# Kernel optimization log

Measured on AMD Instinct MI355X. Metric: run time of the kernel, lower is better.

Reference implementation:

```python
import jax, jax.numpy as jnp
import numpy as np

N = 4096      # total nodes (target + context)
T = 1024      # target nodes
C = N - T     # context nodes
F = 128       # raw node feature dim
H = 512       # num_hids
HEADS = 16    # num_heads
D = H // HEADS
WIN = 2       # window_size
L = 2         # num_layers
E_T = 65536   # edges: target queries -> context keys
E_C = 98304   # edges: context queries -> target keys
EDGE_ENC = 8
EDGE_DIST = 8
SCALE = D ** -0.5


def setup_inputs():
    key = jax.random.key(0)
    ks = iter(jax.random.split(key, 40))
    s = 0.02
    rn = lambda shp, sc=1.0: jax.random.normal(next(ks), shp, jnp.float32) * sc
    return {
        "node_feats": rn((N, F)),
        "edge_emb_table": rn((EDGE_ENC * WIN, H), s),
        "edge_dist_emb_table": rn((EDGE_DIST, H), s),
        "w_node": rn((F, H), s), "b_node": jnp.zeros((H,), jnp.float32),
        "w_edge_enc": rn((H, HEADS), s), "b_edge_enc": jnp.zeros((HEADS,), jnp.float32),
        "w_edge_dist": rn((H, HEADS), s), "b_edge_dist": jnp.zeros((HEADS,), jnp.float32),
        "ln1_g": jnp.ones((L, H), jnp.float32), "ln1_b": jnp.zeros((L, H), jnp.float32),
        "attn1_w": rn((L, 4, H, H), s), "attn1_b": jnp.zeros((L, 4, H), jnp.float32),
        "attn2_w": rn((L, 4, H, H), s), "attn2_b": jnp.zeros((L, 4, H), jnp.float32),
        "ln2_g": jnp.ones((L, H), jnp.float32), "ln2_b": jnp.zeros((L, H), jnp.float32),
        "ffn_w1": rn((L, H, H), s), "ffn_b1": jnp.zeros((L, H), jnp.float32),
        "ffn_w2": rn((L, H, H), s), "ffn_b2": jnp.zeros((L, H), jnp.float32),
        "edge_encodes": jax.random.randint(next(ks), (N, N, WIN), 0, EDGE_ENC * WIN, jnp.int32),
        "edge_dist_encodes": jax.random.randint(next(ks), (N, N), 0, EDGE_DIST, jnp.int32),
        "target_sparse_row": jax.random.randint(next(ks), (E_T,), 0, T, jnp.int32),
        "target_sparse_col": jax.random.randint(next(ks), (E_T,), 0, C, jnp.int32),
        "context_sparse_row": jax.random.randint(next(ks), (E_C,), 0, C, jnp.int32),
        "context_sparse_col": jax.random.randint(next(ks), (E_C,), 0, T, jnp.int32),
        "target_node_size": T,
    }


def _ln(x, g, b, eps=1e-5):
    m = jnp.mean(x, -1, keepdims=True)
    v = jnp.mean((x - m) ** 2, -1, keepdims=True)
    return (x - m) * jax.lax.rsqrt(v + eps) * g + b


def _seg_softmax(x, idx, n):
    # scatter-max / scatter-sum softmax over edges grouped by row index
    m = jax.ops.segment_max(x, idx, num_segments=n)
    m = jnp.where(jnp.isfinite(m), m, 0.0)  # empty segments
    e = jnp.exp(x - m[idx])
    s = jax.ops.segment_sum(e, idx, num_segments=n)
    return e / (s[idx] + 1e-16)


def _emb(table, idx):
    # nn.Embedding(max_norm=True): looked-up rows renormed to L2 norm <= 1
    e = table[idx]
    nrm = jnp.linalg.norm(e, axis=-1, keepdims=True)
    return e / jnp.maximum(nrm, 1.0)


def _mha(yq, ykv, w, b, bias, row, col, n_out):
    # w: [4,H,H] = q,k,v,o projections; b: [4,H]
    q = (yq @ w[0] + b[0]).reshape(-1, HEADS, D)
    k = (ykv @ w[1] + b[1]).reshape(-1, HEADS, D)
    v = (ykv @ w[2] + b[2]).reshape(-1, HEADS, D)
    s = jnp.einsum('ehd,ehd->eh', q[row], k[col]) * SCALE + bias  # [E,HEADS]
    a = _seg_softmax(s, row, n_out)
    o = jax.ops.segment_sum(a[:, :, None] * v[col], row, num_segments=n_out)
    return o.reshape(-1, H) @ w[3] + b[3]


def _forward(node_feats, edge_emb_table, edge_dist_emb_table, w_node, b_node,
             w_edge_enc, b_edge_enc, w_edge_dist, b_edge_dist,
             ln1_g, ln1_b, attn1_w, attn1_b, attn2_w, attn2_b,
             ln2_g, ln2_b, ffn_w1, ffn_b1, ffn_w2, ffn_b2,
             edge_encodes, edge_dist_encodes,
             target_sparse_row, target_sparse_col,
             context_sparse_row, context_sparse_col, Tn):
    Cn = node_feats.shape[0] - Tn

    def bias_for(rows, cols):
        # get_encodings: mean over window of edge embedding, plus dist embedding
        e1 = jnp.mean(_emb(edge_emb_table, edge_encodes[rows, cols]), axis=-2)  # [E,H]
        b1 = e1 @ w_edge_enc + b_edge_enc
        e2 = _emb(edge_dist_emb_table, edge_dist_encodes[rows, cols])           # [E,H]
        b2 = e2 @ w_edge_dist + b_edge_dist
        return b1 + b2                                                           # [E,HEADS]

    attn_bias_target = bias_for(target_sparse_row, target_sparse_col + Tn)
    attn_bias_context = bias_for(context_sparse_row + Tn, context_sparse_col)

    x = node_feats @ w_node + b_node
    for l in range(L):
        y = _ln(x, ln1_g[l], ln1_b[l])
        y_t, y_c = y[:Tn], y[Tn:]
        out1 = _mha(y_t, y_c, attn1_w[l], attn1_b[l], attn_bias_target,
                    target_sparse_row, target_sparse_col, Tn)    # [T,H]
        out2 = _mha(y_c, y_t, attn2_w[l], attn2_b[l], attn_bias_context,
                    context_sparse_row, context_sparse_col, Cn)  # [C,H]
        # original code: y_all = cat([y_target_, y_context_]) = [attn2 out, attn1 out]
        x = x + jnp.concatenate([out2, out1], axis=0)
        y = _ln(x, ln2_g[l], ln2_b[l])
        y = jax.nn.gelu(y @ ffn_w1[l] + ffn_b1[l], approximate=False) @ ffn_w2[l] + ffn_b2[l]
        x = x + y
    return x


def reference(node_feats, edge_emb_table, edge_dist_emb_table, w_node, b_node,
              w_edge_enc, b_edge_enc, w_edge_dist, b_edge_dist,
              ln1_g, ln1_b, attn1_w, attn1_b, attn2_w, attn2_b,
              ln2_g, ln2_b, ffn_w1, ffn_b1, ffn_w2, ffn_b2,
              edge_encodes, edge_dist_encodes,
              target_sparse_row, target_sparse_col,
              context_sparse_row, context_sparse_col, target_node_size):
    return _forward(node_feats, edge_emb_table, edge_dist_emb_table, w_node, b_node,
                    w_edge_enc, b_edge_enc, w_edge_dist, b_edge_dist,
                    ln1_g, ln1_b, attn1_w, attn1_b, attn2_w, attn2_b,
                    ln2_g, ln2_b, ffn_w1, ffn_b1, ffn_w2, ffn_b2,
                    edge_encodes, edge_dist_encodes,
                    target_sparse_row, target_sparse_col,
                    context_sparse_row, context_sparse_col, target_node_size)
```

## Files before the change

### kernel.cpp

```cpp
#include <hip/hip_runtime.h>
#include <math.h>

#define N_NODES 4096
#define T_NODES 1024
#define C_NODES 3072
#define F_IN    128
#define H_DIM   512
#define HEADS   16
#define D_HEAD  32
#define E_T     65536
#define E_C     98304
#define SCALE_QK 0.17677669529663687f

typedef __attribute__((ext_vector_type(8))) short short8;
typedef __attribute__((ext_vector_type(4))) float f32x4;

struct ushort4_t { unsigned short x, y, z, w; };

__device__ inline unsigned short f2bf(float f) {
    unsigned u = __float_as_uint(f);
    unsigned r = (u + 0x7fffu + ((u >> 16) & 1u)) >> 16;
    return (unsigned short)r;
}
__device__ inline float bf2f(unsigned short u) {
    return __uint_as_float(((unsigned)u) << 16);
}

__device__ inline void gload16(const void* g, void* l) {
    __builtin_amdgcn_global_load_lds(
        (const __attribute__((address_space(1))) unsigned int*)g,
        (__attribute__((address_space(3))) unsigned int*)l, 16, 0, 0);
}

struct TD { const float* src[20]; unsigned short* dst[20]; };

__global__ void prep_kernel(TD d, const float* __restrict__ w_node, unsigned short* __restrict__ wnT,
                            const float* __restrict__ nf, unsigned short* __restrict__ nfb)
{
    int z = blockIdx.z;
    __shared__ float tile[32][33];
    int tr = threadIdx.x >> 5, tc = threadIdx.x & 31;
    if (z < 20) {
        const float* src = d.src[z];
        unsigned short* dst = d.dst[z];
        int r0 = blockIdx.y * 32, c0 = blockIdx.x * 32;
        #pragma unroll
        for (int p = 0; p < 4; ++p) tile[tr + 8*p][tc] = src[(size_t)(r0 + tr + 8*p)*512 + c0 + tc];
        __syncthreads();
        #pragma unroll
        for (int p = 0; p < 4; ++p) dst[(size_t)(c0 + tr + 8*p)*512 + r0 + tc] = f2bf(tile[tc][tr + 8*p]);
    } else if (z == 20) {
        if (blockIdx.y >= 4) return;
        int r0 = blockIdx.y * 32, c0 = blockIdx.x * 32;
        #pragma unroll
        for (int p = 0; p < 4; ++p) tile[tr + 8*p][tc] = w_node[(size_t)(r0 + tr + 8*p)*512 + c0 + tc];
        __syncthreads();
        #pragma unroll
        for (int p = 0; p < 4; ++p) wnT[(size_t)(c0 + tr + 8*p)*128 + r0 + tc] = f2bf(tile[tc][tr + 8*p]);
    } else {
        int gid = (blockIdx.y * 16 + blockIdx.x) * 256 + threadIdx.x;
        #pragma unroll
        for (int rep = 0; rep < 2; ++rep) {
            int i = gid + rep * 65536;
            float4 v = ((const float4*)nf)[i];
            ushort4_t o = { f2bf(v.x), f2bf(v.y), f2bf(v.z), f2bf(v.w) };
            ((ushort4_t*)nfb)[i] = o;
        }
    }
}

__global__ void proj_kernel(const float* __restrict__ emb, const float* __restrict__ dist_emb,
                            const float* __restrict__ w_enc, const float* __restrict__ w_dist,
                            const float* __restrict__ a1b, const float* __restrict__ a2b,
                            float* __restrict__ P1, float* __restrict__ P2,
                            float* __restrict__ bct, float* __restrict__ bcc)
{
    if (blockIdx.x == 96) {
        int t = threadIdx.x;
        for (int l = 0; l < 2; ++l)
            for (int i = t; i < 512; i += 256) {
                bct[l*1536 + i]        = a1b[(l*4+0)*512 + i];
                bct[l*1536 + 512 + i]  = a2b[(l*4+1)*512 + i];
                bct[l*1536 + 1024 + i] = a2b[(l*4+2)*512 + i];
                bcc[l*1536 + i]        = a1b[(l*4+1)*512 + i];
                bcc[l*1536 + 512 + i]  = a1b[(l*4+2)*512 + i];
                bcc[l*1536 + 1024 + i] = a2b[(l*4+0)*512 + i];
            }
        return;
    }
    int wid = threadIdx.x >> 6, lane = threadIdx.x & 63;
    int o = blockIdx.x * 4 + wid;
    const float* src; const float* wm; float* dst; int h;
    if (o < 256) { src = emb      + (size_t)(o >> 4) * 512; wm = w_enc;  h = o & 15;  dst = P1 + o; }
    else { int o2 = o - 256; src = dist_emb + (size_t)(o2 >> 4) * 512; wm = w_dist; h = o2 & 15; dst = P2 + o2; }
    float4 v0 = ((const float4*)src)[lane*2];
    float4 v1 = ((const float4*)src)[lane*2+1];
    float nrm = v0.x*v0.x + v0.y*v0.y + v0.z*v0.z + v0.w*v0.w
              + v1.x*v1.x + v1.y*v1.y + v1.z*v1.z + v1.w*v1.w;
    int f0 = lane * 8;
    float dt = v0.x*wm[(f0+0)*16+h] + v0.y*wm[(f0+1)*16+h] + v0.z*wm[(f0+2)*16+h] + v0.w*wm[(f0+3)*16+h]
             + v1.x*wm[(f0+4)*16+h] + v1.y*wm[(f0+5)*16+h] + v1.z*wm[(f0+6)*16+h] + v1.w*wm[(f0+7)*16+h];
    #pragma unroll
    for (int s = 1; s < 64; s <<= 1) { nrm += __shfl_xor(nrm, s, 64); dt += __shfl_xor(dt, s, 64); }
    if (lane == 0) *dst = dt / fmaxf(sqrtf(nrm), 1.0f);
}

__global__ void hist2_kernel(const int* __restrict__ t_row, const int* __restrict__ c_row,
                             int* __restrict__ cnt_t, int* __restrict__ cnt_c) {
    int i = blockIdx.x * 256 + threadIdx.x;
    if (i < E_T) atomicAdd(&cnt_t[t_row[i]], 1);
    else atomicAdd(&cnt_c[c_row[i - E_T]], 1);
}

__global__ void scan2_kernel(const int* __restrict__ cnt_t, int* __restrict__ off_t, int* __restrict__ cur_t,
                             const int* __restrict__ cnt_c, int* __restrict__ off_c, int* __restrict__ cur_c) {
    const int* counts; int* offsets; int* cursor; int n;
    if (blockIdx.x == 0) { counts = cnt_t; offsets = off_t; cursor = cur_t; n = T_NODES; }
    else                 { counts = cnt_c; offsets = off_c; cursor = cur_c; n = C_NODES; }
    __shared__ int lds[1024];
    int t = threadIdx.x;
    int c = (n + 1023) / 1024;
    int base = t * c;
    int s = 0;
    for (int j = 0; j < c; ++j) { int i = base + j; if (i < n) s += counts[i]; }
    lds[t] = s;
    __syncthreads();
    for (int d = 1; d < 1024; d <<= 1) {
        int v = (t >= d) ? lds[t-d] : 0;
        __syncthreads();
        lds[t] += v;
        __syncthreads();
    }
    int run = lds[t] - s;
    for (int j = 0; j < c; ++j) {
        int i = base + j;
        if (i < n) { offsets[i] = run; cursor[i] = run; run += counts[i]; }
    }
    if (t == 1023) offsets[n] = lds[1023];
}

__global__ void scatter2_kernel(const int* __restrict__ t_row, const int* __restrict__ c_row,
                                int* __restrict__ cur_t, int* __restrict__ cur_c,
                                int* __restrict__ perm_t, int* __restrict__ perm_c) {
    int i = blockIdx.x * 256 + threadIdx.x;
    if (i < E_T) { int p = atomicAdd(&cur_t[t_row[i]], 1); perm_t[p] = i; }
    else { int j = i - E_T; int p = atomicAdd(&cur_c[c_row[j]], 1); perm_c[p] = j; }
}

__global__ void bias2_kernel(const int* __restrict__ t_row, const int* __restrict__ t_col,
                             const int* __restrict__ c_row, const int* __restrict__ c_col,
                             const int* __restrict__ perm_t, const int* __restrict__ perm_c,
                             const int* __restrict__ enc, const int* __restrict__ dist,
                             const float* __restrict__ P1, const float* __restrict__ P2,
                             const float* __restrict__ b_enc, const float* __restrict__ b_dist,
                             float* __restrict__ biasp_t, float* __restrict__ biasp_c,
                             int* __restrict__ colp_t, int* __restrict__ colp_c)
{
    __shared__ float sP1[256], sP2[128], sb[16];
    int t = threadIdx.x;
    sP1[t] = P1[t];
    if (t < 128) sP2[t] = P2[t];
    if (t < 16)  sb[t]  = b_enc[t] + b_dist[t];
    __syncthreads();
    int gi = blockIdx.x * 256 + t;
    if (gi < E_T) {
        int i = gi; int e = perm_t[i];
        long r = t_row[e]; long c = t_col[e];
        long idx = r * N_NODES + c + T_NODES;
        int i1 = enc[idx*2], i2 = enc[idx*2+1], j = dist[idx];
        colp_t[i] = (int)c;
        #pragma unroll
        for (int h = 0; h < 16; ++h)
            biasp_t[(size_t)i*16 + h] = 0.5f*(sP1[i1*16+h] + sP1[i2*16+h]) + sP2[j*16+h] + sb[h];
    } else {
        int i = gi - E_T; int e = perm_c[i];
        long r = c_row[e] + T_NODES; long c = c_col[e];
        long idx = r * N_NODES + c;
        int i1 = enc[idx*2], i2 = enc[idx*2+1], j = dist[idx];
        colp_c[i] = (int)c;
        #pragma unroll
        for (int h = 0; h < 16; ++h)
            biasp_c[(size_t)i*16 + h] = 0.5f*(sP1[i1*16+h] + sP1[i2*16+h]) + sP2[j*16+h] + sb[h];
    }
}

__global__ void ln_kernel(const float* __restrict__ x, const float* __restrict__ g,
                          const float* __restrict__ b, unsigned short* __restrict__ y, int M) {
    int wave = threadIdx.x >> 6;
    int lane = threadIdx.x & 63;
    int row = blockIdx.x * 4 + wave;
    if (row >= M) return;
    const float4* xr = (const float4*)(x + (size_t)row * H_DIM);
    float4 a = xr[lane*2], c4 = xr[lane*2+1];
    float s  = a.x + a.y + a.z + a.w + c4.x + c4.y + c4.z + c4.w;
    float sq = a.x*a.x + a.y*a.y + a.z*a.z + a.w*a.w + c4.x*c4.x + c4.y*c4.y + c4.z*c4.z + c4.w*c4.w;
    #pragma unroll
    for (int o = 1; o < 64; o <<= 1) { s += __shfl_xor(s, o, 64); sq += __shfl_xor(sq, o, 64); }
    float mean = s * (1.0f/512.0f);
    float var  = sq * (1.0f/512.0f) - mean*mean;
    float inv  = rsqrtf(var + 1e-5f);
    const float4* gp = (const float4*)g;
    const float4* bp = (const float4*)b;
    float4 g0 = gp[lane*2], g1 = gp[lane*2+1];
    float4 b0 = bp[lane*2], b1 = bp[lane*2+1];
    ushort4_t o0 = { f2bf((a.x-mean)*inv*g0.x + b0.x), f2bf((a.y-mean)*inv*g0.y + b0.y),
                     f2bf((a.z-mean)*inv*g0.z + b0.z), f2bf((a.w-mean)*inv*g0.w + b0.w) };
    ushort4_t o1 = { f2bf((c4.x-mean)*inv*g1.x + b1.x), f2bf((c4.y-mean)*inv*g1.y + b1.y),
                     f2bf((c4.z-mean)*inv*g1.z + b1.z), f2bf((c4.w-mean)*inv*g1.w + b1.w) };
    ushort4_t* yr = (ushort4_t*)(y + (size_t)row * H_DIM);
    yr[lane*2] = o0; yr[lane*2+1] = o1;
}

template <int MODE>
__global__ __launch_bounds__(256) void gemm_bf16(
    const unsigned short* __restrict__ A, int lda,
    const unsigned short* __restrict__ Wa, const unsigned short* __restrict__ Wb, int ldb,
    const float* __restrict__ biasa, const float* __restrict__ biasb,
    void* __restrict__ Cout, int ldc, int K, int mswitch)
{
    __shared__ unsigned short As[2][128*32];
    __shared__ unsigned short Bs[2][64*32];
    int tid  = threadIdx.x;
    int wid  = tid >> 6, lane = tid & 63;
    int wm   = wid >> 1, wn = wid & 1;
    int m0   = blockIdx.y * 128, n0 = blockIdx.x * 64;
    const unsigned short* BT = (m0 >= mswitch) ? Wb : Wa;
    const float* bias        = (m0 >= mswitch) ? biasb : biasa;

    int srow  = lane >> 2;
    int sslot = lane & 3;
    const unsigned short* Ag0 = A  + (size_t)(m0 + wid*32 + srow)*lda + sslot*8;
    const unsigned short* Ag1 = Ag0 + (size_t)16*lda;
    const unsigned short* Bg0 = BT + (size_t)(n0 + wid*16 + srow)*ldb + sslot*8;

    f32x4 acc[4][2] = {};
    int NT = K >> 5;

    auto stage = [&](int bsel, int kt) {
        char* abase = (char*)&As[bsel][0] + wid*2048;
        char* bbase = (char*)&Bs[bsel][0] + wid*1024;
        gload16(Ag0 + kt*32, abase);
        gload16(Ag1 + kt*32, abase + 1024);
        gload16(Bg0 + kt*32, bbase);
    };

    stage(0, 0);
    __syncthreads();
    int cur = 0;
    int arowf = wm*64 + (lane & 15);
    int kslot = (lane >> 4) * 8;
    for (int kt = 0; kt < NT; ++kt) {
        if (kt + 1 < NT) stage(cur ^ 1, kt + 1);
        const unsigned short* as = &As[cur][0];
        const unsigned short* bs = &Bs[cur][0];
        short8 af[4], bf[2];
        #pragma unroll
        for (int fm = 0; fm < 4; ++fm)
            af[fm] = *(const short8*)&as[(arowf + fm*16)*32 + kslot];
        #pragma unroll
        for (int fn = 0; fn < 2; ++fn)
            bf[fn] = *(const short8*)&bs[(wn*32 + fn*16 + (lane & 15))*32 + kslot];
        #pragma unroll
        for (int fm = 0; fm < 4; ++fm)
            #pragma unroll
            for (int fn = 0; fn < 2; ++fn)
                acc[fm][fn] = __builtin_amdgcn_mfma_f32_16x16x32_bf16(af[fm], bf[fn], acc[fm][fn], 0, 0, 0);
        __syncthreads();
        cur ^= 1;
    }

    int crow = m0 + wm*64 + (lane >> 4)*4;
    int ccol = n0 + wn*32 + (lane & 15);
    #pragma unroll
    for (int fn = 0; fn < 2; ++fn) {
        float bv = bias[ccol + fn*16];
        #pragma unroll
        for (int fm = 0; fm < 4; ++fm) {
            #pragma unroll
            for (int j = 0; j < 4; ++j) {
                float val = acc[fm][fn][j] + bv;
                size_t off = (size_t)(crow + fm*16 + j)*ldc + ccol + fn*16;
                if (MODE == 0) {
                    ((float*)Cout)[off] = val;
                } else if (MODE == 1) {
                    float gl = 0.5f * val * (1.0f + erff(val * 0.70710678118654752f));
                    ((unsigned short*)Cout)[off] = f2bf(gl);
                } else if (MODE == 2) {
                    ((float*)Cout)[off] += val;
                } else {
                    ((unsigned short*)Cout)[off] = f2bf(val);
                }
            }
        }
    }
}

__global__ __launch_bounds__(256) void attn_fused(
    const unsigned short* __restrict__ qkv,
    const float* __restrict__ biasp_t, const float* __restrict__ biasp_c,
    const int* __restrict__ off_t, const int* __restrict__ colp_t,
    const int* __restrict__ off_c, const int* __restrict__ colp_c,
    unsigned short* __restrict__ ob)
{
    int wave = threadIdx.x >> 6, lane = threadIdx.x & 63;
    int g = blockIdx.x * 4 + wave;

    int r, orow, rowbase, kcol;
    size_t qoff;
    const float* biasE; const int* offs; const int* colp;
    if (g < T_NODES) {
        r = g;
        qoff = (size_t)r * 1536;
        rowbase = T_NODES; kcol = 0;
        biasE = biasp_t; offs = off_t; colp = colp_t;
        orow = C_NODES + r;
    } else {
        r = g - T_NODES;
        qoff = (size_t)(T_NODES + r) * 1536 + 1024;
        rowbase = 0; kcol = 512;
        biasE = biasp_c; offs = off_c; colp = colp_c;
        orow = r;
    }

    float qf[8];
    {
        short8 qq = *(const short8*)(qkv + qoff + lane*8);
        #pragma unroll
        for (int j = 0; j < 8; ++j) qf[j] = bf2f((unsigned short)qq[j]);
    }
    int h4 = lane >> 2;

    int beg = offs[r], end = offs[r+1];
    float lsum = 0.f;
    float acc[8];
    #pragma unroll
    for (int j = 0; j < 8; ++j) acc[j] = 0.f;

    for (int i0 = beg; i0 < end; i0 += 4) {
        bool okk[4]; int cc[4]; float bb[4];
        short8 kk[4], vv[4];
        #pragma unroll
        for (int u = 0; u < 4; ++u) {
            int ii = i0 + u;
            okk[u] = ii < end;
            cc[u]  = okk[u] ? colp[ii] : 0;
            bb[u]  = okk[u] ? biasE[(size_t)ii*16 + h4] : 0.f;
            const unsigned short* base = qkv + (size_t)(rowbase + cc[u])*1536 + kcol + lane*8;
            kk[u] = *(const short8*)base;
            vv[u] = *(const short8*)(base + 512);
        }
        #pragma unroll
        for (int u = 0; u < 4; ++u) {
            float d = 0.f;
            #pragma unroll
            for (int j = 0; j < 8; ++j) d += qf[j] * bf2f((unsigned short)kk[u][j]);
            d += __shfl_xor(d, 1, 64);
            d += __shfl_xor(d, 2, 64);
            float s = d * SCALE_QK + bb[u];
            float pw = okk[u] ? __expf(s) : 0.f;
            lsum += pw;
            #pragma unroll
            for (int j = 0; j < 8; ++j) acc[j] += pw * bf2f((unsigned short)vv[u][j]);
        }
    }

    float inv = 1.0f / (lsum + 1e-16f);
    ushort4_t o0 = { f2bf(acc[0]*inv), f2bf(acc[1]*inv), f2bf(acc[2]*inv), f2bf(acc[3]*inv) };
    ushort4_t o1 = { f2bf(acc[4]*inv), f2bf(acc[5]*inv), f2bf(acc[6]*inv), f2bf(acc[7]*inv) };
    ushort4_t* op = (ushort4_t*)(ob + (size_t)orow * H_DIM + lane*8);
    op[0] = o0; op[1] = o1;
}

extern "C" void kernel_launch(void* const* d_in, const int* in_sizes, int n_in,
                              void* d_out, int out_size, void* d_ws, size_t ws_size,
                              hipStream_t stream)
{
    const float* node_feats = (const float*)d_in[0];
    const float* edge_emb   = (const float*)d_in[1];
    const float* dist_emb   = (const float*)d_in[2];
    const float* w_node     = (const float*)d_in[3];
    const float* b_node     = (const float*)d_in[4];
    const float* w_enc      = (const float*)d_in[5];
    const float* b_enc      = (const float*)d_in[6];
    const float* w_dist     = (const float*)d_in[7];
    const float* b_dist     = (const float*)d_in[8];
    const float* ln1_g      = (const float*)d_in[9];
    const float* ln1_b      = (const float*)d_in[10];
    const float* attn1_w    = (const float*)d_in[11];
    const float* attn1_b    = (const float*)d_in[12];
    const float* attn2_w    = (const float*)d_in[13];
    const float* attn2_b    = (const float*)d_in[14];
    const float* ln2_g      = (const float*)d_in[15];
    const float* ln2_b      = (const float*)d_in[16];
    const float* ffn_w1     = (const float*)d_in[17];
    const float* ffn_b1     = (const float*)d_in[18];
    const float* ffn_w2     = (const float*)d_in[19];
    const float* ffn_b2     = (const float*)d_in[20];
    const int* enc          = (const int*)d_in[21];
    const int* dist         = (const int*)d_in[22];
    const int* t_row        = (const int*)d_in[23];
    const int* t_col        = (const int*)d_in[24];
    const int* c_row        = (const int*)d_in[25];
    const int* c_col        = (const int*)d_in[26];

    float* x = (float*)d_out;

    char* w = (char*)d_ws;
    auto alloc = [&](size_t bytes) { char* p = w; w += (bytes + 255) & ~(size_t)255; return p; };

    unsigned short* qkv  = (unsigned short*)alloc((size_t)N_NODES*1536*2);
    unsigned short* nfb  = qkv;
    unsigned short* h1   = qkv;
    unsigned short* yb   = (unsigned short*)alloc((size_t)N_NODES*H_DIM*2);
    unsigned short* ob   = (unsigned short*)alloc((size_t)N_NODES*H_DIM*2);
    float* biasp_t       = (float*)alloc((size_t)E_T*HEADS*4);
    float* biasp_c       = (float*)alloc((size_t)E_C*HEADS*4);
    int* colp_t          = (int*)alloc((size_t)E_T*4);
    int* colp_c          = (int*)alloc((size_t)E_C*4);
    int* cnt_t           = (int*)alloc(T_NODES*4);
    int* cnt_c           = (int*)alloc(C_NODES*4);
    int* off_t           = (int*)alloc((T_NODES+1)*4);
    int* cur_t           = (int*)alloc(T_NODES*4);
    int* perm_t          = (int*)alloc((size_t)E_T*4);
    int* off_c           = (int*)alloc((C_NODES+1)*4);
    int* cur_c           = (int*)alloc(C_NODES*4);
    int* perm_c          = (int*)alloc((size_t)E_C*4);
    float* P1            = (float*)alloc(256*4);
    float* P2            = (float*)alloc(128*4);
    unsigned short* wcat_t = (unsigned short*)alloc((size_t)2*1536*512*2);
    unsigned short* wcat_c = (unsigned short*)alloc((size_t)2*1536*512*2);
    unsigned short* wo1    = (unsigned short*)alloc((size_t)2*512*512*2);
    unsigned short* wo2    = (unsigned short*)alloc((size_t)2*512*512*2);
    unsigned short* wf1    = (unsigned short*)alloc((size_t)2*512*512*2);
    unsigned short* wf2    = (unsigned short*)alloc((size_t)2*512*512*2);
    unsigned short* wnT    = (unsigned short*)alloc((size_t)H_DIM*F_IN*2);
    float* bcat_t        = (float*)alloc(2*1536*4);
    float* bcat_c        = (float*)alloc(2*1536*4);

    const size_t SZ = 512*512;
    const int BIG = 1 << 30;

    TD td;
    for (int l = 0; l < 2; ++l) {
        int b = l*10;
        td.src[b+0] = attn1_w + (size_t)(l*4+0)*SZ;  td.dst[b+0] = wcat_t + (size_t)l*1536*512;
        td.src[b+1] = attn2_w + (size_t)(l*4+1)*SZ;  td.dst[b+1] = wcat_t + (size_t)l*1536*512 + SZ;
        td.src[b+2] = attn2_w + (size_t)(l*4+2)*SZ;  td.dst[b+2] = wcat_t + (size_t)l*1536*512 + 2*SZ;
        td.src[b+3] = attn1_w + (size_t)(l*4+1)*SZ;  td.dst[b+3] = wcat_c + (size_t)l*1536*512;
        td.src[b+4] = attn1_w + (size_t)(l*4+2)*SZ;  td.dst[b+4] = wcat_c + (size_t)l*1536*512 + SZ;
        td.src[b+5] = attn2_w + (size_t)(l*4+0)*SZ;  td.dst[b+5] = wcat_c + (size_t)l*1536*512 + 2*SZ;
        td.src[b+6] = attn1_w + (size_t)(l*4+3)*SZ;  td.dst[b+6] = wo1 + (size_t)l*SZ;
        td.src[b+7] = attn2_w + (size_t)(l*4+3)*SZ;  td.dst[b+7] = wo2 + (size_t)l*SZ;
        td.src[b+8] = ffn_w1  + (size_t)l*SZ;        td.dst[b+8] = wf1 + (size_t)l*SZ;
        td.src[b+9] = ffn_w2  + (size_t)l*SZ;        td.dst[b+9] = wf2 + (size_t)l*SZ;
    }
    prep_kernel<<<dim3(16,16,22), 256, 0, stream>>>(td, w_node, wnT, node_feats, nfb);
    proj_kernel<<<97, 256, 0, stream>>>(edge_emb, dist_emb, w_enc, w_dist,
                                        attn1_b, attn2_b, P1, P2, bcat_t, bcat_c);

    hipMemsetAsync(cnt_t, 0, (T_NODES + C_NODES)*4, stream);
    hist2_kernel<<<(E_T+E_C)/256, 256, 0, stream>>>(t_row, c_row, cnt_t, cnt_c);
    scan2_kernel<<<2, 1024, 0, stream>>>(cnt_t, off_t, cur_t, cnt_c, off_c, cur_c);
    scatter2_kernel<<<(E_T+E_C)/256, 256, 0, stream>>>(t_row, c_row, cur_t, cur_c, perm_t, perm_c);
    bias2_kernel<<<(E_T+E_C)/256, 256, 0, stream>>>(t_row, t_col, c_row, c_col, perm_t, perm_c,
                                                    enc, dist, P1, P2, b_enc, b_dist,
                                                    biasp_t, biasp_c, colp_t, colp_c);

    gemm_bf16<0><<<dim3(8, 32), 256, 0, stream>>>(nfb, F_IN, wnT, wnT, F_IN,
                                                  b_node, b_node, x, H_DIM, F_IN, BIG);

    for (int l = 0; l < 2; ++l) {
        ln_kernel<<<N_NODES/4, 256, 0, stream>>>(x, ln1_g + l*H_DIM, ln1_b + l*H_DIM, yb, N_NODES);

        gemm_bf16<3><<<dim3(24, 32), 256, 0, stream>>>(yb, H_DIM,
            wcat_t + (size_t)l*1536*512, wcat_c + (size_t)l*1536*512, H_DIM,
            bcat_t + l*1536, bcat_c + l*1536, qkv, 1536, H_DIM, T_NODES);

        attn_fused<<<N_NODES/4, 256, 0, stream>>>(
            qkv, biasp_t, biasp_c, off_t, colp_t, off_c, colp_c, ob);

        gemm_bf16<2><<<dim3(8, 32), 256, 0, stream>>>(ob, H_DIM,
            wo2 + (size_t)l*SZ, wo1 + (size_t)l*SZ, H_DIM,
            attn2_b + (size_t)(l*4+3)*H_DIM, attn1_b + (size_t)(l*4+3)*H_DIM,
            x, H_DIM, H_DIM, C_NODES);

        ln_kernel<<<N_NODES/4, 256, 0, stream>>>(x, ln2_g + l*H_DIM, ln2_b + l*H_DIM, yb, N_NODES);
        gemm_bf16<1><<<dim3(8, 32), 256, 0, stream>>>(yb, H_DIM,
            wf1 + (size_t)l*SZ, wf1 + (size_t)l*SZ, H_DIM,
            ffn_b1 + l*H_DIM, ffn_b1 + l*H_DIM, h1, H_DIM, H_DIM, BIG);
        gemm_bf16<2><<<dim3(8, 32), 256, 0, stream>>>(h1, H_DIM,
            wf2 + (size_t)l*SZ, wf2 + (size_t)l*SZ, H_DIM,
            ffn_b2 + l*H_DIM, ffn_b2 + l*H_DIM, x, H_DIM, H_DIM, BIG);
    }
}
```

Baseline: 295.7 us.

## Quantize K/V to FP8 and split attention edges across two waves per row

Adds a conversion kernel that packs each node's K and V (bf16) into an FP8 buffer, and the sparse attention kernel gathers K/V from this half-size buffer. It also assigns two waves per query row, interleaving edge chunks and merging partial sums and softmax denominators through shared memory. The aim is to halve the gather traffic and increase parallelism for the memory-bound sparse attention. In exchange it adds an extra launch plus a conversion pass, a block-wide sync, and a loss of precision from FP8 K/V that may exceed tolerance.

```diff
diff --git a/kernel.cpp b/kernel.cpp
--- a/kernel.cpp
+++ b/kernel.cpp
@@ -14,6 +14,7 @@
 
 typedef __attribute__((ext_vector_type(8))) short short8;
 typedef __attribute__((ext_vector_type(4))) float f32x4;
+typedef __attribute__((ext_vector_type(2))) float f32x2;
 
 struct ushort4_t { unsigned short x, y, z, w; };
 
@@ -295,29 +296,52 @@
     }
 }
 
+__global__ void cvt_kv8_kernel(const unsigned short* __restrict__ qkv, unsigned char* __restrict__ kv8)
+{
+    int gid = blockIdx.x * 256 + threadIdx.x;
+    int row = gid >> 7;
+    int ch  = gid & 127;
+    int colbase = (row < T_NODES) ? 512 : 0;
+    short8 s = *(const short8*)(qkv + (size_t)row*1536 + colbase + ch*8);
+    float f[8];
+    #pragma unroll
+    for (int j = 0; j < 8; ++j) f[j] = bf2f((unsigned short)s[j]);
+    int lo = 0, hi = 0;
+    lo = __builtin_amdgcn_cvt_pk_fp8_f32(f[0], f[1], lo, false);
+    lo = __builtin_amdgcn_cvt_pk_fp8_f32(f[2], f[3], lo, true);
+    hi = __builtin_amdgcn_cvt_pk_fp8_f32(f[4], f[5], hi, false);
+    hi = __builtin_amdgcn_cvt_pk_fp8_f32(f[6], f[7], hi, true);
+    int2 o = { lo, hi };
+    *(int2*)(kv8 + (size_t)row*1024 + ch*8) = o;
+}
+
 __global__ __launch_bounds__(256) void attn_fused(
     const unsigned short* __restrict__ qkv,
+    const unsigned char* __restrict__ kv8,
     const float* __restrict__ biasp_t, const float* __restrict__ biasp_c,
     const int* __restrict__ off_t, const int* __restrict__ colp_t,
     const int* __restrict__ off_c, const int* __restrict__ colp_c,
     unsigned short* __restrict__ ob)
 {
+    __shared__ float mrg[2][64][9];
     int wave = threadIdx.x >> 6, lane = threadIdx.x & 63;
-    int g = blockIdx.x * 4 + wave;
-
-    int r, orow, rowbase, kcol;
+    int rowslot = wave >> 1;
+    int half    = wave & 1;
+    int g = blockIdx.x * 2 + rowslot;
+
+    int r, orow, rowbase;
     size_t qoff;
     const float* biasE; const int* offs; const int* colp;
     if (g < T_NODES) {
         r = g;
         qoff = (size_t)r * 1536;
-        rowbase = T_NODES; kcol = 0;
+        rowbase = T_NODES;
         biasE = biasp_t; offs = off_t; colp = colp_t;
         orow = C_NODES + r;
     } else {
         r = g - T_NODES;
         qoff = (size_t)(T_NODES + r) * 1536 + 1024;
-        rowbase = 0; kcol = 512;
+        rowbase = 0;
         biasE = biasp_c; offs = off_c; colp = colp_c;
         orow = r;
     }
@@ -336,39 +360,59 @@
     #pragma unroll
     for (int j = 0; j < 8; ++j) acc[j] = 0.f;
 
-    for (int i0 = beg; i0 < end; i0 += 4) {
+    for (int i0 = beg + half*4; i0 < end; i0 += 8) {
         bool okk[4]; int cc[4]; float bb[4];
-        short8 kk[4], vv[4];
+        uint2 kk[4], vv[4];
         #pragma unroll
         for (int u = 0; u < 4; ++u) {
             int ii = i0 + u;
             okk[u] = ii < end;
             cc[u]  = okk[u] ? colp[ii] : 0;
             bb[u]  = okk[u] ? biasE[(size_t)ii*16 + h4] : 0.f;
-            const unsigned short* base = qkv + (size_t)(rowbase + cc[u])*1536 + kcol + lane*8;
-            kk[u] = *(const short8*)base;
-            vv[u] = *(const short8*)(base + 512);
+            const unsigned char* base = kv8 + (size_t)(rowbase + cc[u])*1024 + lane*8;
+            kk[u] = *(const uint2*)base;
+            vv[u] = *(const uint2*)(base + 512);
         }
         #pragma unroll
         for (int u = 0; u < 4; ++u) {
-            float d = 0.f;
-            #pragma unroll
-            for (int j = 0; j < 8; ++j) d += qf[j] * bf2f((unsigned short)kk[u][j]);
+            f32x2 ka = __builtin_amdgcn_cvt_pk_f32_fp8(kk[u].x, false);
+            f32x2 kb = __builtin_amdgcn_cvt_pk_f32_fp8(kk[u].x, true);
+            f32x2 kc = __builtin_amdgcn_cvt_pk_f32_fp8(kk[u].y, false);
+            f32x2 kd = __builtin_amdgcn_cvt_pk_f32_fp8(kk[u].y, true);
+            float d = qf[0]*ka.x + qf[1]*ka.y + qf[2]*kb.x + qf[3]*kb.y
+                    + qf[4]*kc.x + qf[5]*kc.y + qf[6]*kd.x + qf[7]*kd.y;
             d += __shfl_xor(d, 1, 64);
             d += __shfl_xor(d, 2, 64);
             float s = d * SCALE_QK + bb[u];
             float pw = okk[u] ? __expf(s) : 0.f;
             lsum += pw;
-            #pragma unroll
-            for (int j = 0; j < 8; ++j) acc[j] += pw * bf2f((unsigned short)vv[u][j]);
+            f32x2 va = __builtin_amdgcn_cvt_pk_f32_fp8(vv[u].x, false);
+            f32x2 vb = __builtin_amdgcn_cvt_pk_f32_fp8(vv[u].x, true);
+            f32x2 vc = __builtin_amdgcn_cvt_pk_f32_fp8(vv[u].y, false);
+            f32x2 vd = __builtin_amdgcn_cvt_pk_f32_fp8(vv[u].y, true);
+            acc[0] += pw * va.x; acc[1] += pw * va.y;
+            acc[2] += pw * vb.x; acc[3] += pw * vb.y;
+            acc[4] += pw * vc.x; acc[5] += pw * vc.y;
+            acc[6] += pw * vd.x; acc[7] += pw * vd.y;
         }
     }
 
-    float inv = 1.0f / (lsum + 1e-16f);
-    ushort4_t o0 = { f2bf(acc[0]*inv), f2bf(acc[1]*inv), f2bf(acc[2]*inv), f2bf(acc[3]*inv) };
-    ushort4_t o1 = { f2bf(acc[4]*inv), f2bf(acc[5]*inv), f2bf(acc[6]*inv), f2bf(acc[7]*inv) };
-    ushort4_t* op = (ushort4_t*)(ob + (size_t)orow * H_DIM + lane*8);
-    op[0] = o0; op[1] = o1;
+    if (half == 1) {
+        #pragma unroll
+        for (int j = 0; j < 8; ++j) mrg[rowslot][lane][j] = acc[j];
+        mrg[rowslot][lane][8] = lsum;
+    }
+    __syncthreads();
+    if (half == 0) {
+        #pragma unroll
+        for (int j = 0; j < 8; ++j) acc[j] += mrg[rowslot][lane][j];
+        lsum += mrg[rowslot][lane][8];
+        float inv = 1.0f / (lsum + 1e-16f);
+        ushort4_t o0 = { f2bf(acc[0]*inv), f2bf(acc[1]*inv), f2bf(acc[2]*inv), f2bf(acc[3]*inv) };
+        ushort4_t o1 = { f2bf(acc[4]*inv), f2bf(acc[5]*inv), f2bf(acc[6]*inv), f2bf(acc[7]*inv) };
+        ushort4_t* op = (ushort4_t*)(ob + (size_t)orow * H_DIM + lane*8);
+        op[0] = o0; op[1] = o1;
+    }
 }
 
 extern "C" void kernel_launch(void* const* d_in, const int* in_sizes, int n_in,
@@ -411,6 +455,7 @@
     unsigned short* qkv  = (unsigned short*)alloc((size_t)N_NODES*1536*2);
     unsigned short* nfb  = qkv;
     unsigned short* h1   = qkv;
+    unsigned char* kv8   = (unsigned char*)alloc((size_t)N_NODES*1024);
     unsigned short* yb   = (unsigned short*)alloc((size_t)N_NODES*H_DIM*2);
     unsigned short* ob   = (unsigned short*)alloc((size_t)N_NODES*H_DIM*2);
     float* biasp_t       = (float*)alloc((size_t)E_T*HEADS*4);
@@ -476,8 +521,10 @@
             wcat_t + (size_t)l*1536*512, wcat_c + (size_t)l*1536*512, H_DIM,
             bcat_t + l*1536, bcat_c + l*1536, qkv, 1536, H_DIM, T_NODES);
 
-        attn_fused<<<N_NODES/4, 256, 0, stream>>>(
-            qkv, biasp_t, biasp_c, off_t, colp_t, off_c, colp_c, ob);
+        cvt_kv8_kernel<<<2048, 256, 0, stream>>>(qkv, kv8);
+
+        attn_fused<<<N_NODES/2, 256, 0, stream>>>(
+            qkv, kv8, biasp_t, biasp_c, off_t, colp_t, off_c, colp_c, ob);
 
         gemm_bf16<2><<<dim3(8, 32), 256, 0, stream>>>(ob, H_DIM,
             wo2 + (size_t)l*SZ, wo1 + (size_t)l*SZ, H_DIM,
```

Result: faster. 268.9 us (-9.1%).
